# Kernel optimization log

Hardware: AMD Instinct MI355X
Metric: run time of the kernel (lower is better)

The kernel has to match this reference:

```python
import jax, jax.numpy as jnp
import numpy as np

GROUPS = 32
EPS = 1e-6


def group_norm(x, scale, bias):
    B, C, H, W = x.shape
    xg = x.reshape(B, GROUPS, C // GROUPS, H, W)
    mean = xg.mean(axis=(2, 3, 4), keepdims=True)
    var = xg.var(axis=(2, 3, 4), keepdims=True)
    xg = (xg - mean) * jax.lax.rsqrt(var + EPS)
    x = xg.reshape(B, C, H, W)
    return x * scale[None, :, None, None] + bias[None, :, None, None]


def conv1x1(x, w, b):
    # x: [B,C,H,W], w: [O,C], b: [O]
    return jnp.einsum('bchw,oc->bohw', x, w) + b[None, :, None, None]


def setup_inputs() -> dict:
    key = jax.random.key(0)
    ks = jax.random.split(key, 6)
    B, C, H, W = 8, 256, 64, 64
    s = 1.0 / np.sqrt(C)
    return {
        'x': jax.random.normal(ks[0], (B, C, H, W), dtype=jnp.float32),
        'gn_scale': jnp.ones((C,), dtype=jnp.float32),
        'gn_bias': jnp.zeros((C,), dtype=jnp.float32),
        'wq': jax.random.normal(ks[1], (C, C), dtype=jnp.float32) * s,
        'bq': jnp.zeros((C,), dtype=jnp.float32),
        'wk': jax.random.normal(ks[2], (C, C), dtype=jnp.float32) * s,
        'bk': jnp.zeros((C,), dtype=jnp.float32),
        'wv': jax.random.normal(ks[3], (C, C), dtype=jnp.float32) * s,
        'bv': jnp.zeros((C,), dtype=jnp.float32),
        'wo': jax.random.normal(ks[4], (C, C), dtype=jnp.float32) * s,
        'bo': jnp.zeros((C,), dtype=jnp.float32),
    }


def reference(x, gn_scale, gn_bias, wq, bq, wk, bk, wv, bv, wo, bo):
    skip = x
    h = group_norm(x, gn_scale, gn_bias)
    B, C, H, W = h.shape
    N = H * W
    q = conv1x1(h, wq, bq).reshape(B, C, N)  # [B,C,N]
    k = conv1x1(h, wk, bk).reshape(B, C, N)
    v = conv1x1(h, wv, bv).reshape(B, C, N)
    # scores[b,i,j] = sum_c q[b,c,i] k[b,c,j] / sqrt(C)
    scores = jnp.einsum('bci,bcj->bij', q, k) / jnp.sqrt(jnp.float32(C))
    a = jax.nn.softmax(scores, axis=2)  # softmax over keys j
    # z[b,c,i] = sum_j v[b,c,j] a[b,i,j]
    z = jnp.einsum('bcj,bij->bci', v, a).reshape(B, C, H, W)
    z = conv1x1(z, wo, bo)
    return skip + z
```

## Files before the change

### kernel.cpp

```cpp
#include <hip/hip_runtime.h>
#include <math.h>

typedef __bf16 bf16;
typedef __bf16 bf16x8 __attribute__((ext_vector_type(8)));
typedef __bf16 bf16x4 __attribute__((ext_vector_type(4)));
typedef float  f32x4  __attribute__((ext_vector_type(4)));
typedef float  f32x16 __attribute__((ext_vector_type(16)));
typedef unsigned int u32;
typedef unsigned char u8;
typedef u32 u32x2 __attribute__((ext_vector_type(2)));
typedef u32 u32x4 __attribute__((ext_vector_type(4)));
typedef int  i32x8 __attribute__((ext_vector_type(8)));

#define MFMA(a, b, c)   __builtin_amdgcn_mfma_f32_16x16x32_bf16((a), (b), (c), 0, 0, 0)
#define MFMAS(a, b, c)                                                           \
  __builtin_amdgcn_mfma_scale_f32_32x32x64_f8f6f4((a), (b), (c), 0, 0,           \
                                                  0, 0x7f7f7f7f, 0, 0x7f7f7f7f)

#define GLOAD_LDS16(g, l)                                                        \
  __builtin_amdgcn_global_load_lds(                                              \
      (const __attribute__((address_space(1))) void*)(g),                        \
      (__attribute__((address_space(3))) void*)(l), 16, 0, 0)

static constexpr int B_ = 8, C_ = 256, N_ = 4096;
static constexpr float QSCALE = 0.09016844005556021f;
static constexpr float PBIAS  = 2.0f;

static constexpr size_t HT_OFF = 0;
static constexpr size_t QT_OFF = 16777216;
static constexpr size_t KT_OFF = 25165824;
static constexpr size_t V_OFF  = 33554432;
static constexpr size_t WQ_OFF = 41943040;
static constexpr size_t WK_OFF = WQ_OFF + 131072;
static constexpr size_t WV_OFF = WK_OFF + 131072;
static constexpr size_t WO_OFF = WV_OFF + 131072;
static constexpr size_t LS_OFF = WO_OFF + 131072;
static constexpr size_t ZN2_OFF = LS_OFF + 524288;
static constexpr size_t PART_ELEMS = (size_t)B_ * C_ * N_;

__global__ __launch_bounds__(512) void gn_kernel(
    const float* __restrict__ x, const float* __restrict__ gsc, const float* __restrict__ gbi,
    bf16* __restrict__ hT,
    const float* __restrict__ wq, const float* __restrict__ wk,
    const float* __restrict__ wv, const float* __restrict__ wo,
    bf16* __restrict__ oq, bf16* __restrict__ ok, bf16* __restrict__ ov, bf16* __restrict__ oo) {
  int b = blockIdx.x >> 5, g = blockIdx.x & 31, c0 = g * 8;
  int t = threadIdx.x;
  if (t < 256) {
    int i = blockIdx.x * 256 + t;
    oq[i] = (bf16)wq[i];
    ok[i] = (bf16)wk[i];
    ov[i] = (bf16)wv[i];
    oo[i] = (bf16)wo[i];
  }
  const float* base = x + ((size_t)(b * C_ + c0)) * N_;
  __shared__ bf16 xl[32768];
  float s = 0.f, ss = 0.f;
  const f32x4* b4 = (const f32x4*)base;
#pragma unroll
  for (int p = 0; p < 16; p++) {
    int u = t + p * 512;
    f32x4 v = b4[u];
    s  += v[0] + v[1] + v[2] + v[3];
    ss += v[0] * v[0] + v[1] * v[1] + v[2] * v[2] + v[3] * v[3];
    bf16x4 xv;
#pragma unroll
    for (int e = 0; e < 4; e++) xv[e] = (bf16)v[e];
    *(bf16x4*)(xl + u * 4) = xv;
  }
#pragma unroll
  for (int off = 1; off < 64; off <<= 1) {
    s  += __shfl_xor(s, off);
    ss += __shfl_xor(ss, off);
  }
  __shared__ float red[16];
  if ((t & 63) == 0) { red[(t >> 6) * 2] = s; red[(t >> 6) * 2 + 1] = ss; }
  __syncthreads();
  s = 0.f; ss = 0.f;
#pragma unroll
  for (int r = 0; r < 8; r++) { s += red[r * 2]; ss += red[r * 2 + 1]; }
  float mean = s * (1.f / 32768.f);
  float var  = ss * (1.f / 32768.f) - mean * mean;
  float rstd = rsqrtf(var + 1e-6f);
  float aa[8], bb[8];
#pragma unroll
  for (int cc = 0; cc < 8; cc++) {
    aa[cc] = rstd * gsc[c0 + cc];
    bb[cc] = gbi[c0 + cc] - mean * aa[cc];
  }
#pragma unroll
  for (int ii = 0; ii < 8; ii++) {
    int i = t + ii * 512;
    bf16x8 o;
#pragma unroll
    for (int cc = 0; cc < 8; cc++) o[cc] = (bf16)((float)xl[cc * 4096 + i] * aa[cc] + bb[cc]);
    *(bf16x8*)(hT + ((size_t)(b * N_ + i)) * C_ + c0) = o;
  }
}

__global__ __launch_bounds__(256) void qkv_kernel(
    const bf16* __restrict__ hT,
    const bf16* __restrict__ wqb, const bf16* __restrict__ wkb, const bf16* __restrict__ wvb,
    const float* __restrict__ bq, const float* __restrict__ bk, const float* __restrict__ bv,
    u8* __restrict__ qT8, u8* __restrict__ kT8, u8* __restrict__ v8) {
  int b = blockIdx.x >> 6, i0 = (blockIdx.x & 63) << 6;
  int t = threadIdx.x, w = t >> 6, lane = t & 63, quad = lane >> 4, l15 = lane & 15;
  __shared__ bf16 hl[64 * 264];
  __shared__ __align__(16) u8 ep[16384];
#pragma unroll
  for (int p = 0; p < 8; p++) {
    int u = t + p * 256, r = u >> 5, c16 = u & 31;
    *(bf16x8*)(hl + r * 264 + c16 * 8) =
        *(const bf16x8*)(hT + ((size_t)(b * N_ + i0 + r)) * C_ + c16 * 8);
  }
  __syncthreads();
  int cw0 = w * 64;

  f32x4 aq[4][4], ak[4][4];
#pragma unroll
  for (int a = 0; a < 4; a++)
#pragma unroll
    for (int bb2 = 0; bb2 < 4; bb2++) { aq[a][bb2] = (f32x4){0.f,0.f,0.f,0.f}; ak[a][bb2] = (f32x4){0.f,0.f,0.f,0.f}; }
  for (int kc = 0; kc < 8; kc++) {
    bf16x8 hb[4];
#pragma unroll
    for (int it = 0; it < 4; it++)
      hb[it] = *(const bf16x8*)(hl + (it * 16 + l15) * 264 + kc * 32 + quad * 8);
#pragma unroll
    for (int ct = 0; ct < 4; ct++) {
      bf16x8 wqf = *(const bf16x8*)(wqb + ((size_t)(cw0 + ct * 16 + l15)) * C_ + kc * 32 + quad * 8);
      bf16x8 wkf = *(const bf16x8*)(wkb + ((size_t)(cw0 + ct * 16 + l15)) * C_ + kc * 32 + quad * 8);
#pragma unroll
      for (int it = 0; it < 4; it++) {
        aq[ct][it] = MFMA(wqf, hb[it], aq[ct][it]);
        ak[ct][it] = MFMA(wkf, hb[it], ak[ct][it]);
      }
    }
  }

#pragma unroll
  for (int ct = 0; ct < 4; ct++)
#pragma unroll
    for (int it = 0; it < 4; it++) {
      int c4 = cw0 + ct * 16 + quad * 4;
      int il = it * 16 + l15;
      f32x4 bq4 = *(const f32x4*)(bq + c4);
      float qv[4];
#pragma unroll
      for (int r = 0; r < 4; r++) qv[r] = (aq[ct][it][r] + bq4[r]) * (QSCALE * 4.0f);
      u32 qd = (u32)__builtin_amdgcn_cvt_pk_fp8_f32(qv[0], qv[1], 0, false);
      qd = (u32)__builtin_amdgcn_cvt_pk_fp8_f32(qv[2], qv[3], (int)qd, true);
      *(u32*)(ep + il * 256 + ((((c4 >> 4) ^ (il & 15)) << 4) | (c4 & 12))) = qd;
    }
  __syncthreads();
#pragma unroll
  for (int p = 0; p < 4; p++) {
    int u = p * 256 + t, il = u >> 4, ch = u & 15;
    *(u32x4*)(qT8 + ((size_t)(b * N_ + i0 + il)) * C_ + ch * 16) =
        *(const u32x4*)(ep + il * 256 + (((ch ^ (il & 15)) << 4)));
  }
  __syncthreads();

#pragma unroll
  for (int ct = 0; ct < 4; ct++)
#pragma unroll
    for (int it = 0; it < 4; it++) {
      int c4 = cw0 + ct * 16 + quad * 4;
      int il = it * 16 + l15;
      f32x4 bk4 = *(const f32x4*)(bk + c4);
      float kv[4];
#pragma unroll
      for (int r = 0; r < 4; r++) kv[r] = (ak[ct][it][r] + bk4[r]) * 0.25f;
      u32 kd = (u32)__builtin_amdgcn_cvt_pk_fp8_f32(kv[0], kv[1], 0, false);
      kd = (u32)__builtin_amdgcn_cvt_pk_fp8_f32(kv[2], kv[3], (int)kd, true);
      *(u32*)(ep + il * 256 + ((((c4 >> 4) ^ (il & 15)) << 4) | (c4 & 12))) = kd;
    }
  __syncthreads();
#pragma unroll
  for (int p = 0; p < 4; p++) {
    int u = p * 256 + t, il = u >> 4, ch = u & 15;
    *(u32x4*)(kT8 + ((size_t)(b * N_ + i0 + il)) * C_ + ch * 16) =
        *(const u32x4*)(ep + il * 256 + (((ch ^ (il & 15)) << 4)));
  }

  f32x4 av[4][4];
#pragma unroll
  for (int a = 0; a < 4; a++)
#pragma unroll
    for (int bb2 = 0; bb2 < 4; bb2++) av[a][bb2] = (f32x4){0.f,0.f,0.f,0.f};
  for (int kc = 0; kc < 8; kc++) {
    bf16x8 ha[4];
#pragma unroll
    for (int it = 0; it < 4; it++)
      ha[it] = *(const bf16x8*)(hl + (it * 16 + l15) * 264 + kc * 32 + quad * 8);
#pragma unroll
    for (int ct = 0; ct < 4; ct++) {
      bf16x8 wvf = *(const bf16x8*)(wvb + ((size_t)(cw0 + ct * 16 + l15)) * C_ + kc * 32 + quad * 8);
#pragma unroll
      for (int it = 0; it < 4; it++) av[it][ct] = MFMA(ha[it], wvf, av[it][ct]);
    }
  }
  __syncthreads();

#pragma unroll
  for (int it = 0; it < 4; it++)
#pragma unroll
    for (int ct = 0; ct < 4; ct++) {
      int cl = cw0 + ct * 16 + l15;
      float bvc = bv[cl];
      float vv4[4];
#pragma unroll
      for (int r = 0; r < 4; r++) vv4[r] = av[it][ct][r] + bvc;
      u32 vd = (u32)__builtin_amdgcn_cvt_pk_fp8_f32(vv4[0], vv4[1], 0, false);
      vd = (u32)__builtin_amdgcn_cvt_pk_fp8_f32(vv4[2], vv4[3], (int)vd, true);
      *(u32*)(ep + cl * 64 + ((((it ^ (cl & 3)) << 4)) | (quad * 4))) = vd;
    }
  __syncthreads();
#pragma unroll
  for (int p = 0; p < 4; p++) {
    int u = p * 256 + t, cl = u >> 2, io = u & 3;
    *(u32x4*)(v8 + ((size_t)(b * C_ + cl)) * N_ + i0 + io * 16) =
        *(const u32x4*)(ep + cl * 64 + (((io ^ (cl & 3)) << 4)));
  }
}

__global__ __launch_bounds__(256, 2) void attn_kernel(
    const u8* __restrict__ qT8, const u8* __restrict__ kT8, const u8* __restrict__ v8,
    bf16* __restrict__ zn0, bf16* __restrict__ znR, float* __restrict__ lsum) {
  constexpr int NJT = 32;
  int blk = blockIdx.x;
  int sp = blk >> 8;
  int b = blk & 7;
  int i0 = ((blk >> 3) & 31) << 7;
  int t = threadIdx.x, w = t >> 6, lane = t & 63;
  int r31 = lane & 31, h = lane >> 5;
  __shared__ __align__(16) u8 lds8[4 * 16384];

  int iw = i0 + w * 32;
  const u8* qrow = qT8 + ((size_t)(b * N_ + iw + r31)) * C_ + h * 32;
  i32x8 qB[4];
#pragma unroll
  for (int m = 0; m < 4; m++) qB[m] = *(const i32x8*)(qrow + m * 64);

  f32x16 of[8];
#pragma unroll
  for (int ct = 0; ct < 8; ct++)
#pragma unroll
    for (int e = 0; e < 16; e++) of[ct][e] = 0.f;
  float lacc = 0.f;

  int ks = r31 & 7;
  int kr_off = lane >> 4;
  int kc_pos = lane & 15;
  int vr_off = lane >> 2;
  int vc_pos = lane & 3;
  int spBase = sp * 2048;

  auto stageK = [&](int jts, u8* kb) {
    int j0s = spBase + jts * 64;
#pragma unroll
    for (int p = 0; p < 4; p++) {
      int idx = w * 4 + p;
      int r = idx * 4 + kr_off;
      int chunk = kc_pos ^ (r & 7);
      GLOAD_LDS16(kT8 + ((size_t)(b * N_ + j0s + r)) * C_ + chunk * 16, kb + idx * 1024);
    }
  };
  auto stageV = [&](int jts, u8* vb) {
    int j0s = spBase + jts * 64;
#pragma unroll
    for (int p = 0; p < 4; p++) {
      int idx = w * 4 + p;
      int c = idx * 16 + vr_off;
      int chunk = vc_pos ^ ((c >> 1) & 3);
      GLOAD_LDS16(v8 + ((size_t)(b * C_ + c)) * N_ + j0s + chunk * 16, vb + idx * 1024);
    }
  };

  stageK(0, lds8);
  stageV(0, lds8 + 32768);

  if (__popc(blk) & 1) __builtin_amdgcn_s_sleep(48);

  i32x8 pPrev;

  for (int jt = 0; jt < NJT; jt++) {
    stageK(jt < NJT - 1 ? jt + 1 : jt, lds8 + (((jt + 1) & 1) << 14));
    asm volatile("s_waitcnt vmcnt(8)" ::: "memory");
    __builtin_amdgcn_s_barrier();
    const u8* kTl = lds8 + ((jt & 1) << 14);
    const u8* vbp = lds8 + 32768 + (((jt + 1) & 1) << 14);

    f32x16 st0;
#pragma unroll
    for (int e = 0; e < 16; e++) st0[e] = -PBIAS;
    {
      const u8* krow = kTl + r31 * 256;
      __builtin_amdgcn_s_setprio(1);
#pragma unroll
      for (int m = 0; m < 4; m++) {
        int cd = m * 4 + h * 2;
        union { i32x8 v; u32x4 h4[2]; } kf;
        kf.h4[0] = *(const u32x4*)(krow + ((cd ^ ks) * 16));
        kf.h4[1] = *(const u32x4*)(krow + (((cd + 1) ^ ks) * 16));
        st0 = MFMAS(kf.v, qB[m], st0);
      }
    }
    if (jt) {
#pragma unroll
      for (int ct = 0; ct < 8; ct++) {
        int c = ct * 32 + r31;
        int vs = (c >> 1) & 3;
        const u8* vrow = vbp + c * 64;
        union { i32x8 v; u32x4 h4[2]; } vB;
        vB.h4[0] = *(const u32x4*)(vrow + (((2 * h) ^ vs) * 16));
        vB.h4[1] = *(const u32x4*)(vrow + (((2 * h + 1) ^ vs) * 16));
        of[ct] = MFMAS(pPrev, vB.v, of[ct]);
      }
    }
    __builtin_amdgcn_s_setprio(0);
    u32 PG0[4], PG1[4];
#pragma unroll
    for (int b4 = 0; b4 < 4; b4++) {
      float p0 = __builtin_amdgcn_exp2f(st0[b4 * 4 + 0]);
      float p1 = __builtin_amdgcn_exp2f(st0[b4 * 4 + 1]);
      float p2 = __builtin_amdgcn_exp2f(st0[b4 * 4 + 2]);
      float p3 = __builtin_amdgcn_exp2f(st0[b4 * 4 + 3]);
      lacc += (p0 + p1) + (p2 + p3);
      u32 d = (u32)__builtin_amdgcn_cvt_pk_fp8_f32(p0, p1, 0, false);
      d = (u32)__builtin_amdgcn_cvt_pk_fp8_f32(p2, p3, (int)d, true);
      PG0[b4] = d;
    }
    f32x16 st1;
#pragma unroll
    for (int e = 0; e < 16; e++) st1[e] = -PBIAS;
    {
      const u8* krow = kTl + (32 + r31) * 256;
      __builtin_amdgcn_s_setprio(1);
#pragma unroll
      for (int m = 0; m < 4; m++) {
        int cd = m * 4 + h * 2;
        union { i32x8 v; u32x4 h4[2]; } kf;
        kf.h4[0] = *(const u32x4*)(krow + ((cd ^ ks) * 16));
        kf.h4[1] = *(const u32x4*)(krow + (((cd + 1) ^ ks) * 16));
        st1 = MFMAS(kf.v, qB[m], st1);
      }
      __builtin_amdgcn_s_setprio(0);
    }
#pragma unroll
    for (int b4 = 0; b4 < 4; b4++) {
      float p0 = __builtin_amdgcn_exp2f(st1[b4 * 4 + 0]);
      float p1 = __builtin_amdgcn_exp2f(st1[b4 * 4 + 1]);
      float p2 = __builtin_amdgcn_exp2f(st1[b4 * 4 + 2]);
      float p3 = __builtin_amdgcn_exp2f(st1[b4 * 4 + 3]);
      lacc += (p0 + p1) + (p2 + p3);
      u32 d = (u32)__builtin_amdgcn_cvt_pk_fp8_f32(p0, p1, 0, false);
      d = (u32)__builtin_amdgcn_cvt_pk_fp8_f32(p2, p3, (int)d, true);
      PG1[b4] = d;
    }
#pragma unroll
    for (int b4 = 0; b4 < 4; b4++) {
      u32x2 rr = __builtin_amdgcn_permlane32_swap(PG0[b4], PG1[b4], false, false);
      pPrev[2 * b4]     = (int)rr[0];
      pPrev[2 * b4 + 1] = (int)rr[1];
    }

    __builtin_amdgcn_s_barrier();
    if (jt < NJT - 1) stageV(jt + 1, lds8 + 32768 + (((jt + 1) & 1) << 14));
  }

  asm volatile("s_waitcnt vmcnt(0)" ::: "memory");
  __builtin_amdgcn_s_barrier();
  {
    const u8* vbp = lds8 + 32768 + (((NJT - 1) & 1) << 14);
#pragma unroll
    for (int ct = 0; ct < 8; ct++) {
      int c = ct * 32 + r31;
      int vs = (c >> 1) & 3;
      const u8* vrow = vbp + c * 64;
      union { i32x8 v; u32x4 h4[2]; } vB;
      vB.h4[0] = *(const u32x4*)(vrow + (((2 * h) ^ vs) * 16));
      vB.h4[1] = *(const u32x4*)(vrow + (((2 * h + 1) ^ vs) * 16));
      of[ct] = MFMAS(pPrev, vB.v, of[ct]);
    }
  }

  lacc += __shfl_xor(lacc, 32);
  if (h == 0)
    lsum[((size_t)(sp * 8 + b)) * N_ + iw + r31] = lacc;
  bf16* zn = (sp == 0) ? zn0 : znR;
#pragma unroll
  for (int ct = 0; ct < 8; ct++) {
    int c = ct * 32 + r31;
#pragma unroll
    for (int g = 0; g < 4; g++) {
      bf16x4 zv;
#pragma unroll
      for (int e = 0; e < 4; e++) zv[e] = (bf16)of[ct][g * 4 + e];
      int i4 = iw + 8 * g + 4 * h;
      *(bf16x4*)(zn + ((size_t)(b * C_ + c)) * N_ + i4) = zv;
    }
  }
}

__global__ __launch_bounds__(256) void combine_kernel(
    const bf16* __restrict__ zn0, const bf16* __restrict__ znR,
    const float* __restrict__ lsum,
    const bf16* __restrict__ wob, const float* __restrict__ bo,
    const float* __restrict__ x, float* __restrict__ out) {
  int b = blockIdx.x >> 6, i0 = (blockIdx.x & 63) << 6;
  int t = threadIdx.x, w = t >> 6, lane = t & 63, quad = lane >> 4, l15 = lane & 15;
  __shared__ bf16 zl[64 * 266];
  __shared__ float linv[64];

  if (t < 64) {
    size_t ii = (size_t)b * N_ + i0 + t;
    linv[t] = 1.f / (lsum[ii] + lsum[ii + (size_t)8 * N_]);
  }
  __syncthreads();

#pragma unroll
  for (int p = 0; p < 16; p++) {
    int u = t + p * 256, c = u >> 4, ii = (u & 15) * 4;
    size_t base = ((size_t)(b * C_ + c)) * N_ + i0 + ii;
    bf16x4 z0 = *(const bf16x4*)(zn0 + base);
    bf16x4 z1 = *(const bf16x4*)(znR + base);
#pragma unroll
    for (int e = 0; e < 4; e++)
      zl[(ii + e) * 266 + c] = (bf16)(((float)z0[e] + (float)z1[e]) * linv[ii + e]);
  }
  __syncthreads();

  f32x4 oa[4][4];
#pragma unroll
  for (int a = 0; a < 4; a++)
#pragma unroll
    for (int bb2 = 0; bb2 < 4; bb2++) oa[a][bb2] = (f32x4){0.f, 0.f, 0.f, 0.f};
  for (int kc = 0; kc < 8; kc++) {
    bf16x8 za[4];
#pragma unroll
    for (int it = 0; it < 4; it++)
      za[it] = *(const bf16x8*)(zl + (it * 16 + l15) * 266 + kc * 32 + quad * 8);
#pragma unroll
    for (int ctl = 0; ctl < 4; ctl++) {
      bf16x8 wf = *(const bf16x8*)(wob + ((size_t)(w * 64 + ctl * 16 + l15)) * C_ + kc * 32 + quad * 8);
#pragma unroll
      for (int it = 0; it < 4; it++) oa[ctl][it] = MFMA(za[it], wf, oa[ctl][it]);
    }
  }
#pragma unroll
  for (int ctl = 0; ctl < 4; ctl++)
#pragma unroll
    for (int it = 0; it < 4; it++) {
      int c = w * 64 + ctl * 16 + l15;
      size_t base = ((size_t)(b * C_ + c)) * N_ + i0 + it * 16 + quad * 4;
      f32x4 xs = *(const f32x4*)(x + base);
      float boc = bo[c];
      f32x4 o4;
#pragma unroll
      for (int r = 0; r < 4; r++) o4[r] = oa[ctl][it][r] + boc + xs[r];
      *(f32x4*)(out + base) = o4;
    }
}

extern "C" void kernel_launch(void* const* d_in, const int* in_sizes, int n_in,
                              void* d_out, int out_size, void* d_ws, size_t ws_size,
                              hipStream_t stream) {
  const float* x   = (const float*)d_in[0];
  const float* gsc = (const float*)d_in[1];
  const float* gbi = (const float*)d_in[2];
  const float* wq  = (const float*)d_in[3];
  const float* bq  = (const float*)d_in[4];
  const float* wk  = (const float*)d_in[5];
  const float* bk  = (const float*)d_in[6];
  const float* wv  = (const float*)d_in[7];
  const float* bv  = (const float*)d_in[8];
  const float* wo  = (const float*)d_in[9];
  const float* bo  = (const float*)d_in[10];

  char* ws = (char*)d_ws;
  bf16* hT   = (bf16*)(ws + HT_OFF);
  u8*   qT8  = (u8*)(ws + QT_OFF);
  u8*   kT8  = (u8*)(ws + KT_OFF);
  u8*   v8   = (u8*)(ws + V_OFF);
  bf16* wqb  = (bf16*)(ws + WQ_OFF);
  bf16* wkb  = (bf16*)(ws + WK_OFF);
  bf16* wvb  = (bf16*)(ws + WV_OFF);
  bf16* wob  = (bf16*)(ws + WO_OFF);
  float* lsum = (float*)(ws + LS_OFF);
  bf16* zn0  = (bf16*)(ws + HT_OFF);
  bf16* znR  = (bf16*)(ws + ZN2_OFF);

  gn_kernel<<<256, 512, 0, stream>>>(x, gsc, gbi, hT, wq, wk, wv, wo, wqb, wkb, wvb, wob);
  qkv_kernel<<<512, 256, 0, stream>>>(hT, wqb, wkb, wvb, bq, bk, bv, qT8, kT8, v8);
  attn_kernel<<<512, 256, 0, stream>>>(qT8, kT8, v8, zn0, znR, lsum);
  combine_kernel<<<512, 256, 0, stream>>>(zn0, znR, lsum, wob, bo, x, (float*)d_out);
}
```

Baseline: 243.5 us.

## Split QKV projection into per-matrix passes with smaller row tiles

The fused QKV kernel, which computed Q, K and V for 64 rows per block, is split so each block handles one projection (Q, K or V) for 32 rows. The grid grows from 512 to 3072 blocks, and launch bounds ask for higher occupancy, to spread work across the GPU and cut per-block register and LDS pressure. In exchange, each hT tile is now loaded three times, once per pass, and weight loads are reused across fewer rows.

```diff
diff --git a/kernel.cpp b/kernel.cpp
--- a/kernel.cpp
+++ b/kernel.cpp
@@ -25,6 +25,7 @@
 static constexpr int B_ = 8, C_ = 256, N_ = 4096;
 static constexpr float QSCALE = 0.09016844005556021f;
 static constexpr float PBIAS  = 2.0f;
+
 
 static constexpr size_t HT_OFF = 0;
 static constexpr size_t QT_OFF = 16777216;
@@ -98,17 +99,22 @@
   }
 }
 
-__global__ __launch_bounds__(256) void qkv_kernel(
+__global__ __launch_bounds__(256, 5) void qkv_kernel(
     const bf16* __restrict__ hT,
     const bf16* __restrict__ wqb, const bf16* __restrict__ wkb, const bf16* __restrict__ wvb,
     const float* __restrict__ bq, const float* __restrict__ bk, const float* __restrict__ bv,
     u8* __restrict__ qT8, u8* __restrict__ kT8, u8* __restrict__ v8) {
-  int b = blockIdx.x >> 6, i0 = (blockIdx.x & 63) << 6;
+  int blk = blockIdx.x;
+  int pass = blk >> 10;
+  int bi = blk & 1023;
+  int b = bi >> 7, i0 = (bi & 127) << 5;
   int t = threadIdx.x, w = t >> 6, lane = t & 63, quad = lane >> 4, l15 = lane & 15;
-  __shared__ bf16 hl[64 * 264];
-  __shared__ __align__(16) u8 ep[16384];
-#pragma unroll
-  for (int p = 0; p < 8; p++) {
+  __shared__ bf16 hl[32 * 264];
+  __shared__ __align__(16) u8 ep[8192];
+  const bf16* wsel = (pass == 0) ? wqb : (pass == 1) ? wkb : wvb;
+
+#pragma unroll
+  for (int p = 0; p < 4; p++) {
     int u = t + p * 256, r = u >> 5, c16 = u & 31;
     *(bf16x8*)(hl + r * 264 + c16 * 8) =
         *(const bf16x8*)(hT + ((size_t)(b * N_ + i0 + r)) * C_ + c16 * 8);
@@ -116,111 +122,86 @@
   __syncthreads();
   int cw0 = w * 64;
 
-  f32x4 aq[4][4], ak[4][4];
-#pragma unroll
-  for (int a = 0; a < 4; a++)
-#pragma unroll
-    for (int bb2 = 0; bb2 < 4; bb2++) { aq[a][bb2] = (f32x4){0.f,0.f,0.f,0.f}; ak[a][bb2] = (f32x4){0.f,0.f,0.f,0.f}; }
-  for (int kc = 0; kc < 8; kc++) {
-    bf16x8 hb[4];
-#pragma unroll
-    for (int it = 0; it < 4; it++)
-      hb[it] = *(const bf16x8*)(hl + (it * 16 + l15) * 264 + kc * 32 + quad * 8);
-#pragma unroll
-    for (int ct = 0; ct < 4; ct++) {
-      bf16x8 wqf = *(const bf16x8*)(wqb + ((size_t)(cw0 + ct * 16 + l15)) * C_ + kc * 32 + quad * 8);
-      bf16x8 wkf = *(const bf16x8*)(wkb + ((size_t)(cw0 + ct * 16 + l15)) * C_ + kc * 32 + quad * 8);
-#pragma unroll
-      for (int it = 0; it < 4; it++) {
-        aq[ct][it] = MFMA(wqf, hb[it], aq[ct][it]);
-        ak[ct][it] = MFMA(wkf, hb[it], ak[ct][it]);
-      }
-    }
-  }
-
-#pragma unroll
-  for (int ct = 0; ct < 4; ct++)
-#pragma unroll
-    for (int it = 0; it < 4; it++) {
-      int c4 = cw0 + ct * 16 + quad * 4;
-      int il = it * 16 + l15;
-      f32x4 bq4 = *(const f32x4*)(bq + c4);
-      float qv[4];
-#pragma unroll
-      for (int r = 0; r < 4; r++) qv[r] = (aq[ct][it][r] + bq4[r]) * (QSCALE * 4.0f);
-      u32 qd = (u32)__builtin_amdgcn_cvt_pk_fp8_f32(qv[0], qv[1], 0, false);
-      qd = (u32)__builtin_amdgcn_cvt_pk_fp8_f32(qv[2], qv[3], (int)qd, true);
-      *(u32*)(ep + il * 256 + ((((c4 >> 4) ^ (il & 15)) << 4) | (c4 & 12))) = qd;
-    }
-  __syncthreads();
-#pragma unroll
-  for (int p = 0; p < 4; p++) {
-    int u = p * 256 + t, il = u >> 4, ch = u & 15;
-    *(u32x4*)(qT8 + ((size_t)(b * N_ + i0 + il)) * C_ + ch * 16) =
-        *(const u32x4*)(ep + il * 256 + (((ch ^ (il & 15)) << 4)));
-  }
-  __syncthreads();
-
-#pragma unroll
-  for (int ct = 0; ct < 4; ct++)
-#pragma unroll
-    for (int it = 0; it < 4; it++) {
-      int c4 = cw0 + ct * 16 + quad * 4;
-      int il = it * 16 + l15;
-      f32x4 bk4 = *(const f32x4*)(bk + c4);
-      float kv[4];
-#pragma unroll
-      for (int r = 0; r < 4; r++) kv[r] = (ak[ct][it][r] + bk4[r]) * 0.25f;
-      u32 kd = (u32)__builtin_amdgcn_cvt_pk_fp8_f32(kv[0], kv[1], 0, false);
-      kd = (u32)__builtin_amdgcn_cvt_pk_fp8_f32(kv[2], kv[3], (int)kd, true);
-      *(u32*)(ep + il * 256 + ((((c4 >> 4) ^ (il & 15)) << 4) | (c4 & 12))) = kd;
-    }
-  __syncthreads();
-#pragma unroll
-  for (int p = 0; p < 4; p++) {
-    int u = p * 256 + t, il = u >> 4, ch = u & 15;
-    *(u32x4*)(kT8 + ((size_t)(b * N_ + i0 + il)) * C_ + ch * 16) =
-        *(const u32x4*)(ep + il * 256 + (((ch ^ (il & 15)) << 4)));
-  }
-
-  f32x4 av[4][4];
-#pragma unroll
-  for (int a = 0; a < 4; a++)
-#pragma unroll
-    for (int bb2 = 0; bb2 < 4; bb2++) av[a][bb2] = (f32x4){0.f,0.f,0.f,0.f};
-  for (int kc = 0; kc < 8; kc++) {
-    bf16x8 ha[4];
-#pragma unroll
-    for (int it = 0; it < 4; it++)
-      ha[it] = *(const bf16x8*)(hl + (it * 16 + l15) * 264 + kc * 32 + quad * 8);
-#pragma unroll
-    for (int ct = 0; ct < 4; ct++) {
-      bf16x8 wvf = *(const bf16x8*)(wvb + ((size_t)(cw0 + ct * 16 + l15)) * C_ + kc * 32 + quad * 8);
-#pragma unroll
-      for (int it = 0; it < 4; it++) av[it][ct] = MFMA(ha[it], wvf, av[it][ct]);
-    }
-  }
-  __syncthreads();
-
-#pragma unroll
-  for (int it = 0; it < 4; it++)
-#pragma unroll
-    for (int ct = 0; ct < 4; ct++) {
-      int cl = cw0 + ct * 16 + l15;
-      float bvc = bv[cl];
-      float vv4[4];
-#pragma unroll
-      for (int r = 0; r < 4; r++) vv4[r] = av[it][ct][r] + bvc;
-      u32 vd = (u32)__builtin_amdgcn_cvt_pk_fp8_f32(vv4[0], vv4[1], 0, false);
-      vd = (u32)__builtin_amdgcn_cvt_pk_fp8_f32(vv4[2], vv4[3], (int)vd, true);
-      *(u32*)(ep + cl * 64 + ((((it ^ (cl & 3)) << 4)) | (quad * 4))) = vd;
-    }
-  __syncthreads();
-#pragma unroll
-  for (int p = 0; p < 4; p++) {
-    int u = p * 256 + t, cl = u >> 2, io = u & 3;
-    *(u32x4*)(v8 + ((size_t)(b * C_ + cl)) * N_ + i0 + io * 16) =
-        *(const u32x4*)(ep + cl * 64 + (((io ^ (cl & 3)) << 4)));
+  if (pass < 2) {
+    const float* bias = (pass == 0) ? bq : bk;
+    float scale = (pass == 0) ? (QSCALE * 4.0f) : 0.25f;
+    u8* outp = (pass == 0) ? qT8 : kT8;
+    f32x4 acc[4][2];
+#pragma unroll
+    for (int a = 0; a < 4; a++)
+#pragma unroll
+      for (int bb2 = 0; bb2 < 2; bb2++) acc[a][bb2] = (f32x4){0.f, 0.f, 0.f, 0.f};
+    for (int kc = 0; kc < 8; kc++) {
+      bf16x8 hb[2];
+#pragma unroll
+      for (int it = 0; it < 2; it++)
+        hb[it] = *(const bf16x8*)(hl + (it * 16 + l15) * 264 + kc * 32 + quad * 8);
+#pragma unroll
+      for (int ct = 0; ct < 4; ct++) {
+        bf16x8 wf = *(const bf16x8*)(wsel + ((size_t)(cw0 + ct * 16 + l15)) * C_ + kc * 32 + quad * 8);
+#pragma unroll
+        for (int it = 0; it < 2; it++) acc[ct][it] = MFMA(wf, hb[it], acc[ct][it]);
+      }
+    }
+#pragma unroll
+    for (int ct = 0; ct < 4; ct++)
+#pragma unroll
+      for (int it = 0; it < 2; it++) {
+        int c4 = cw0 + ct * 16 + quad * 4;
+        int il = it * 16 + l15;
+        f32x4 b4v = *(const f32x4*)(bias + c4);
+        float qv[4];
+#pragma unroll
+        for (int r = 0; r < 4; r++) qv[r] = (acc[ct][it][r] + b4v[r]) * scale;
+        u32 qd = (u32)__builtin_amdgcn_cvt_pk_fp8_f32(qv[0], qv[1], 0, false);
+        qd = (u32)__builtin_amdgcn_cvt_pk_fp8_f32(qv[2], qv[3], (int)qd, true);
+        *(u32*)(ep + il * 256 + ((((c4 >> 4) ^ (il & 15)) << 4) | (c4 & 12))) = qd;
+      }
+    __syncthreads();
+#pragma unroll
+    for (int p = 0; p < 2; p++) {
+      int u = p * 256 + t, il = u >> 4, ch = u & 15;
+      *(u32x4*)(outp + ((size_t)(b * N_ + i0 + il)) * C_ + ch * 16) =
+          *(const u32x4*)(ep + il * 256 + (((ch ^ (il & 15)) << 4)));
+    }
+  } else {
+    f32x4 acc[2][4];
+#pragma unroll
+    for (int a = 0; a < 2; a++)
+#pragma unroll
+      for (int bb2 = 0; bb2 < 4; bb2++) acc[a][bb2] = (f32x4){0.f, 0.f, 0.f, 0.f};
+    for (int kc = 0; kc < 8; kc++) {
+      bf16x8 hb[2];
+#pragma unroll
+      for (int it = 0; it < 2; it++)
+        hb[it] = *(const bf16x8*)(hl + (it * 16 + l15) * 264 + kc * 32 + quad * 8);
+#pragma unroll
+      for (int ct = 0; ct < 4; ct++) {
+        bf16x8 wf = *(const bf16x8*)(wsel + ((size_t)(cw0 + ct * 16 + l15)) * C_ + kc * 32 + quad * 8);
+#pragma unroll
+        for (int it = 0; it < 2; it++) acc[it][ct] = MFMA(hb[it], wf, acc[it][ct]);
+      }
+    }
+#pragma unroll
+    for (int it = 0; it < 2; it++)
+#pragma unroll
+      for (int ct = 0; ct < 4; ct++) {
+        int cl = cw0 + ct * 16 + l15;
+        float bvc = bv[cl];
+        float vv4[4];
+#pragma unroll
+        for (int r = 0; r < 4; r++) vv4[r] = acc[it][ct][r] + bvc;
+        u32 vd = (u32)__builtin_amdgcn_cvt_pk_fp8_f32(vv4[0], vv4[1], 0, false);
+        vd = (u32)__builtin_amdgcn_cvt_pk_fp8_f32(vv4[2], vv4[3], (int)vd, true);
+        *(u32*)(ep + cl * 32 + (((it ^ (cl & 1)) << 4) | (quad * 4))) = vd;
+      }
+    __syncthreads();
+#pragma unroll
+    for (int p = 0; p < 2; p++) {
+      int u = p * 256 + t, cl = u >> 1, io = u & 1;
+      *(u32x4*)(v8 + ((size_t)(b * C_ + cl)) * N_ + i0 + io * 16) =
+          *(const u32x4*)(ep + cl * 32 + (((io ^ (cl & 1)) << 4)));
+    }
   }
 }
 
@@ -492,7 +473,7 @@
   bf16* znR  = (bf16*)(ws + ZN2_OFF);
 
   gn_kernel<<<256, 512, 0, stream>>>(x, gsc, gbi, hT, wq, wk, wv, wo, wqb, wkb, wvb, wob);
-  qkv_kernel<<<512, 256, 0, stream>>>(hT, wqb, wkb, wvb, bq, bk, bv, qT8, kT8, v8);
+  qkv_kernel<<<3072, 256, 0, stream>>>(hT, wqb, wkb, wvb, bq, bk, bv, qT8, kT8, v8);
   attn_kernel<<<512, 256, 0, stream>>>(qT8, kT8, v8, zn0, znR, lsum);
   combine_kernel<<<512, 256, 0, stream>>>(zn0, znR, lsum, wob, bo, x, (float*)d_out);
 }
```

Result: slower. 262.8 us (+7.9%).
